# Performance work log

Hardware: AMD Instinct MI355X
Metric: run time of the kernel (lower is better)

## Reference

```python
import jax, jax.numpy as jnp
import numpy as np

DIM = 768
HEADS = 12

def setup_inputs() -> dict:
    key = jax.random.key(0)
    k_x, k_qw, k_qb, k_pw, k_pb = jax.random.split(key, 5)
    x = jax.random.normal(k_x, (4, 2048, DIM), dtype=jnp.float32)
    s = 1.0 / np.sqrt(DIM)
    # torch nn.Linear convention: y = x @ W.T + b, W shape [out, in]
    qkv_w = jax.random.uniform(k_qw, (3 * DIM, DIM), jnp.float32, -s, s)
    qkv_b = jax.random.uniform(k_qb, (3 * DIM,), jnp.float32, -s, s)
    proj_w = jax.random.uniform(k_pw, (DIM, DIM), jnp.float32, -s, s)
    proj_b = jax.random.uniform(k_pb, (DIM,), jnp.float32, -s, s)
    return {"x": x, "qkv_w": qkv_w, "qkv_b": qkv_b, "proj_w": proj_w, "proj_b": proj_b}

def reference(x, qkv_w, qkv_b, proj_w, proj_b):
    B, N, C = x.shape
    H = HEADS
    D = C // H
    scale = D ** -0.5
    qkv = x @ qkv_w.T + qkv_b                      # [B, N, 3C]
    qkv = qkv.reshape(B, N, 3, H, D).transpose(2, 0, 3, 1, 4)  # [3, B, H, N, D]
    q, k, v = qkv[0], qkv[1], qkv[2]
    attn = jnp.einsum('bhnd,bhmd->bhnm', q, k) * scale  # [B, H, N, N]
    attn = jax.nn.softmax(attn, axis=-1)           # dropout p=0.0 -> identity
    out = jnp.einsum('bhnm,bhmd->bhnd', attn, v)   # [B, H, N, D]
    out = out.transpose(0, 2, 1, 3).reshape(B, N, C)
    return out @ proj_w.T + proj_b
```

## Files before the change

kernel.cpp:

```cpp
#include <hip/hip_runtime.h>

#define DIM 768
#define HEADS 12
#define HDIM 64
#define BATCH 4
#define SEQ 2048
#define QSCALE 0.1803368787f
#define MFIX 16.0f
#define QKVSZ ((size_t)BATCH * HEADS * SEQ * HDIM)

typedef __bf16 bf16x8 __attribute__((ext_vector_type(8)));
typedef float  f32x4  __attribute__((ext_vector_type(4)));
typedef float  f32x16 __attribute__((ext_vector_type(16)));
typedef unsigned short u16x8 __attribute__((ext_vector_type(8)));
typedef unsigned short ushort_t;

__device__ inline float exp2_hw(float x){
    float r;
    asm("v_exp_f32 %0, %1\n\ts_nop 0" : "=v"(r) : "v"(x));
    return r;
}
__device__ inline unsigned short f2bf(float x){
    unsigned int u = __float_as_uint(x);
    u += 0x7fffu + ((u >> 16) & 1u);
    return (unsigned short)(u >> 16);
}
__device__ inline unsigned int cvtpk(float lo, float hi){
    unsigned int r;
    asm("v_cvt_pk_bf16_f32 %0, %1, %2" : "=v"(r) : "v"(lo), "v"(hi));
    return r;
}
__device__ inline void gload_lds16(const void* g, void* lds) {
    __builtin_amdgcn_global_load_lds(
        (const __attribute__((address_space(1))) void*)g,
        (__attribute__((address_space(3))) void*)lds, 16, 0, 0);
}

__global__ __launch_bounds__(256) void cvt3(
    const float* __restrict__ s0, ushort_t* __restrict__ d0, int v0,
    const float* __restrict__ s1, ushort_t* __restrict__ d1, int v1,
    const float* __restrict__ s2, ushort_t* __restrict__ d2, int v2)
{
    int idx = blockIdx.x * 256 + threadIdx.x;
    const float* s; ushort_t* d;
    if (idx < v0)           { s = s0; d = d0; }
    else if (idx < v0 + v1) { idx -= v0; s = s1; d = d1; }
    else                    { idx -= v0 + v1; s = s2; d = d2; }
    float4 a = *(const float4*)(s + (size_t)idx * 8);
    float4 b = *(const float4*)(s + (size_t)idx * 8 + 4);
    u16x8 p;
    p[0] = f2bf(a.x); p[1] = f2bf(a.y); p[2] = f2bf(a.z); p[3] = f2bf(a.w);
    p[4] = f2bf(b.x); p[5] = f2bf(b.y); p[6] = f2bf(b.z); p[7] = f2bf(b.w);
    *(u16x8*)(d + (size_t)idx * 8) = p;
}

template <int MODE>
__global__ __launch_bounds__(256) void gemm_mfma(
    const ushort_t* __restrict__ A, const ushort_t* __restrict__ W,
    const float* __restrict__ bias, void* __restrict__ outp,
    int M, int N, int K)
{
    __shared__ ushort_t As[128 * 64];
    __shared__ ushort_t Bs[128 * 64];

    const int tid  = threadIdx.x;
    const int lane = tid & 63;
    const int w    = tid >> 6;
    const int l16  = lane & 15;
    const int lg   = lane >> 4;
    const int wm = w >> 1, wn = w & 1;
    const int m0 = blockIdx.y << 7;
    const int n0 = blockIdx.x << 7;

    const int srow = lane >> 3;
    const int clds = lane & 7;
    const int cg   = clds ^ srow;
    const ushort_t* pA = A + (size_t)(m0 + w * 32 + srow) * K + cg * 8;
    const ushort_t* pB = W + (size_t)(n0 + w * 32 + srow) * K + cg * 8;
    ushort_t* lA = As + (w * 32) * 64;
    ushort_t* lB = Bs + (w * 32) * 64;

    f32x4 acc[4][4];
#pragma unroll
    for (int mi = 0; mi < 4; ++mi)
#pragma unroll
        for (int ni = 0; ni < 4; ++ni) acc[mi][ni] = (f32x4){0.f, 0.f, 0.f, 0.f};

    const int s7  = l16 & 7;
    const int ck0 = (lg ^ s7) << 3;
    const int ck1 = ((4 | lg) ^ s7) << 3;
    const int arow = (wm * 64 + l16) * 64;
    const int brow = (wn * 64 + l16) * 64;

    const int KT = K >> 6;
    for (int kt = 0; kt < KT; ++kt) {
        __syncthreads();
        const ushort_t* ga = pA + kt * 64;
        const ushort_t* gb = pB + kt * 64;
#pragma unroll
        for (int j = 0; j < 4; ++j) {
            gload_lds16(ga + (size_t)j * 8 * K, lA + j * 8 * 64);
            gload_lds16(gb + (size_t)j * 8 * K, lB + j * 8 * 64);
        }
        __syncthreads();

        bf16x8 af[2][4], bfr[2][4];
#pragma unroll
        for (int mi = 0; mi < 4; ++mi) {
            af[0][mi] = *(const bf16x8*)(As + arow + mi * 16 * 64 + ck0);
            af[1][mi] = *(const bf16x8*)(As + arow + mi * 16 * 64 + ck1);
        }
#pragma unroll
        for (int ni = 0; ni < 4; ++ni) {
            bfr[0][ni] = *(const bf16x8*)(Bs + brow + ni * 16 * 64 + ck0);
            bfr[1][ni] = *(const bf16x8*)(Bs + brow + ni * 16 * 64 + ck1);
        }
#pragma unroll
        for (int kk = 0; kk < 2; ++kk)
#pragma unroll
            for (int mi = 0; mi < 4; ++mi)
#pragma unroll
                for (int ni = 0; ni < 4; ++ni)
                    acc[mi][ni] = __builtin_amdgcn_mfma_f32_16x16x32_bf16(
                        af[kk][mi], bfr[kk][ni], acc[mi][ni], 0, 0, 0);
    }

#pragma unroll
    for (int ni = 0; ni < 4; ++ni) {
        const int n = n0 + wn * 64 + ni * 16 + l16;
        const float bv = bias[n];
        if (MODE == 0) {
            float* out = (float*)outp;
#pragma unroll
            for (int mi = 0; mi < 4; ++mi)
#pragma unroll
                for (int r = 0; r < 4; ++r) {
                    const int m = m0 + wm * 64 + mi * 16 + lg * 4 + r;
                    out[(size_t)m * N + n] = acc[mi][ni][r] + bv;
                }
        } else {
            ushort_t* out = (ushort_t*)outp;
            const int which = n / DIM;
            const int rem   = n % DIM;
            const int h = rem >> 6;
            const int d = rem & 63;
            if (which < 2) {
                const float sc = (which == 0) ? QSCALE : 1.0f;
                ushort_t* base = out + (size_t)which * QKVSZ;
#pragma unroll
                for (int mi = 0; mi < 4; ++mi)
#pragma unroll
                    for (int r = 0; r < 4; ++r) {
                        const int m = m0 + wm * 64 + mi * 16 + lg * 4 + r;
                        const int b = m >> 11;
                        const int nrow = m & (SEQ - 1);
                        base[((size_t)(b * HEADS + h) * SEQ + nrow) * HDIM + d] =
                            f2bf((acc[mi][ni][r] + bv) * sc);
                    }
            } else {
                ushort_t* base = out + 2 * QKVSZ;
#pragma unroll
                for (int mi = 0; mi < 4; ++mi) {
                    const int m = m0 + wm * 64 + mi * 16 + lg * 4;
                    const int b = m >> 11;
                    const int nrow = m & (SEQ - 1);
                    ushort4 pk;
                    pk.x = f2bf(acc[mi][ni][0] + bv);
                    pk.y = f2bf(acc[mi][ni][1] + bv);
                    pk.z = f2bf(acc[mi][ni][2] + bv);
                    pk.w = f2bf(acc[mi][ni][3] + bv);
                    *(ushort4*)&base[((size_t)(b * HEADS + h) * HDIM + d) * SEQ + nrow] = pk;
                }
            }
        }
    }
}

__global__ __launch_bounds__(256) void flash_attn_mfma(
    const ushort_t* __restrict__ Qg, const ushort_t* __restrict__ Kg,
    const ushort_t* __restrict__ VTg, ushort_t* __restrict__ Og)
{
    __shared__ ushort_t Ks[2][4096];
    __shared__ ushort_t Vs[2][4096];

    const int tid  = threadIdx.x;
    const int lane = tid & 63;
    const int w    = tid >> 6;
    const int l32  = lane & 31;
    const int hi   = lane >> 5;

    const int L   = blockIdx.x;
    const int swz = (L & 7) * 96 + (L >> 3);
    const int bh  = swz >> 4;
    const int qt  = swz & 15;
    const int q0  = qt * 128 + w * 32;

    const ushort_t* Qp  = Qg + ((size_t)bh * SEQ + q0) * HDIM;
    const ushort_t* Kp  = Kg + (size_t)bh * SEQ * HDIM;
    const ushort_t* VTp = VTg + (size_t)bh * HDIM * SEQ;

    bf16x8 qf[4];
#pragma unroll
    for (int kd = 0; kd < 4; ++kd)
        qf[kd] = *(const bf16x8*)(Qp + l32 * HDIM + kd * 16 + hi * 8);

    bf16x8 ones;
    {
        union { bf16x8 v; unsigned int w4[4]; } u;
        u.w4[0] = u.w4[1] = u.w4[2] = u.w4[3] = 0x3F803F80u;
        ones = u.v;
    }

    f32x16 oacc[2], lacc;
#pragma unroll
    for (int nb = 0; nb < 2; ++nb)
#pragma unroll
        for (int r = 0; r < 16; ++r) oacc[nb][r] = 0.f;
#pragma unroll
    for (int r = 0; r < 16; ++r) lacc[r] = 0.f;

    const int srow = lane >> 3;
    const int clds = lane & 7;
    const int cg   = clds ^ srow;
    const int rw   = w * 16 + srow;

    const ushort_t* gk = Kp + (size_t)rw * HDIM + cg * 8;
    const ushort_t* gv = VTp + (size_t)rw * SEQ + cg * 8;
    ushort_t* lk0 = &Ks[0][0] + w * 1024;
    ushort_t* lv0 = &Vs[0][0] + w * 1024;

    auto stage = [&](int buf) {
        ushort_t* lkb = lk0 + (buf << 12);
        ushort_t* lvb = lv0 + (buf << 12);
        gload_lds16(gk, lkb);
        gload_lds16(gk + 8 * HDIM, lkb + 512);
        gload_lds16(gv, lvb);
        gload_lds16(gv + 8 * SEQ, lvb + 512);
    };

    stage(0);
    gk += 64 * HDIM; gv += 64;
    __syncthreads();

    int cur = 0;
    const int NT = SEQ / 64;
    for (int kt = 0; kt < NT; ++kt) {
        if (kt + 1 < NT) {
            stage(cur ^ 1);
            gk += 64 * HDIM; gv += 64;
        }

        const ushort_t* Kb = &Ks[0][0] + (cur << 12);
        const ushort_t* Vb = &Vs[0][0] + (cur << 12);

#pragma unroll
        for (int b = 0; b < 2; ++b) {
            f32x16 sacc;
#pragma unroll
            for (int r = 0; r < 16; ++r) sacc[r] = -MFIX;
            const int arow = b * 32 + l32;
            const int s7   = l32 & 7;
            __builtin_amdgcn_s_setprio(1);
#pragma unroll
            for (int kd = 0; kd < 4; ++kd) {
                bf16x8 kf = *(const bf16x8*)(Kb + arow * 64 + (((kd * 2 + hi) ^ s7) << 3));
                sacc = __builtin_amdgcn_mfma_f32_32x32x16_bf16(kf, qf[kd], sacc, 0, 0, 0);
            }
            __builtin_amdgcn_s_setprio(0);

            float p[16];
#pragma unroll
            for (int r = 0; r < 16; ++r) p[r] = exp2_hw(sacc[r]);

#pragma unroll
            for (int s = 0; s < 2; ++s) {
                unsigned int x0 = cvtpk(p[8 * s + 0], p[8 * s + 1]);
                unsigned int y0 = cvtpk(p[8 * s + 4], p[8 * s + 5]);
                unsigned int x1 = cvtpk(p[8 * s + 2], p[8 * s + 3]);
                unsigned int y1 = cvtpk(p[8 * s + 6], p[8 * s + 7]);
                asm("v_permlane32_swap_b32 %0, %1" : "+v"(x0), "+v"(y0));
                asm("v_permlane32_swap_b32 %0, %1" : "+v"(x1), "+v"(y1));
                union { bf16x8 v; unsigned int w4[4]; } pa;
                pa.w4[0] = x0; pa.w4[1] = x1; pa.w4[2] = y0; pa.w4[3] = y1;
                const int kc = b * 4 + s * 2 + hi;
                __builtin_amdgcn_s_setprio(1);
                lacc = __builtin_amdgcn_mfma_f32_32x32x16_bf16(pa.v, ones, lacc, 0, 0, 0);
#pragma unroll
                for (int nb = 0; nb < 2; ++nb) {
                    int d = nb * 32 + l32;
                    bf16x8 vf = *(const bf16x8*)(Vb + d * 64 + ((kc ^ (d & 7)) << 3));
                    oacc[nb] = __builtin_amdgcn_mfma_f32_32x32x16_bf16(
                        pa.v, vf, oacc[nb], 0, 0, 0);
                }
                __builtin_amdgcn_s_setprio(0);
            }
        }

        __syncthreads();
        cur ^= 1;
    }

    const int b_ = bh / HEADS;
    const int h_ = bh % HEADS;
    ushort_t* Ob = Og + ((size_t)b_ * SEQ + q0) * DIM + h_ * HDIM;
#pragma unroll
    for (int r = 0; r < 16; ++r) {
        int q = (r & 3) + 8 * (r >> 2) + 4 * hi;
        float li = __builtin_amdgcn_rcpf(lacc[r]);
#pragma unroll
        for (int nb = 0; nb < 2; ++nb)
            Ob[(size_t)q * DIM + nb * 32 + l32] = f2bf(oacc[nb][r] * li);
    }
}

extern "C" void kernel_launch(void* const* d_in, const int* in_sizes, int n_in,
                              void* d_out, int out_size, void* d_ws, size_t ws_size,
                              hipStream_t stream)
{
    const float* x      = (const float*)d_in[0];
    const float* qkv_w  = (const float*)d_in[1];
    const float* qkv_b  = (const float*)d_in[2];
    const float* proj_w = (const float*)d_in[3];
    const float* proj_b = (const float*)d_in[4];
    float* out = (float*)d_out;

    ushort_t* qb     = (ushort_t*)d_ws;
    ushort_t* kb     = qb + QKVSZ;
    ushort_t* vtb    = qb + 2 * QKVSZ;
    ushort_t* attn   = qb + 3 * QKVSZ;
    ushort_t* xb     = qb + 4 * QKVSZ;
    ushort_t* qkvwb  = xb + QKVSZ;
    ushort_t* projwb = qkvwb + (size_t)3 * DIM * DIM;

    const int M = BATCH * SEQ;
    const int NX  = M * DIM;
    const int NQW = 3 * DIM * DIM;
    const int NPW = DIM * DIM;

    cvt3<<<dim3((NX + NQW + NPW) / (8 * 256)), dim3(256), 0, stream>>>(
        x, xb, NX / 8, qkv_w, qkvwb, NQW / 8, proj_w, projwb, NPW / 8);

    dim3 g1(3 * DIM / 128, M / 128);
    gemm_mfma<1><<<g1, dim3(256), 0, stream>>>(xb, qkvwb, qkv_b, (void*)qb, M, 3 * DIM, DIM);

    flash_attn_mfma<<<dim3(768), dim3(256), 0, stream>>>(qb, kb, vtb, attn);

    dim3 g3(DIM / 128, M / 128);
    gemm_mfma<0><<<g3, dim3(256), 0, stream>>>(attn, projwb, proj_b, (void*)out, M, DIM, DIM);
}
```

Measured before the change: 146.4 us.

## Split MFMA accumulators into independent chains and compute row sum on VALU

The QK^T MFMA chain now uses two independent accumulators, and the PV accumulation alternates between two accumulator sets, which shortens dependent MFMA chains. The softmax row-sum MFMA against a ones vector is replaced by a VALU sum of the fp32 exponentials, with a cross-half shuffle and a per-row broadcast at the end. This removes one MFMA per PV step and breaks serial accumulator dependencies, at the cost of more accumulator registers that may reduce occupancy. The row sum is now taken from fp32 values rather than bf16-rounded ones, which slightly changes numerics.

```diff
diff --git a/kernel.cpp b/kernel.cpp
--- a/kernel.cpp
+++ b/kernel.cpp
@@ -204,20 +204,12 @@
     for (int kd = 0; kd < 4; ++kd)
         qf[kd] = *(const bf16x8*)(Qp + l32 * HDIM + kd * 16 + hi * 8);
 
-    bf16x8 ones;
-    {
-        union { bf16x8 v; unsigned int w4[4]; } u;
-        u.w4[0] = u.w4[1] = u.w4[2] = u.w4[3] = 0x3F803F80u;
-        ones = u.v;
-    }
-
-    f32x16 oacc[2], lacc;
+    f32x16 oaccA[2], oaccB[2];
 #pragma unroll
     for (int nb = 0; nb < 2; ++nb)
 #pragma unroll
-        for (int r = 0; r < 16; ++r) oacc[nb][r] = 0.f;
-#pragma unroll
-    for (int r = 0; r < 16; ++r) lacc[r] = 0.f;
+        for (int r = 0; r < 16; ++r) { oaccA[nb][r] = 0.f; oaccB[nb][r] = 0.f; }
+    float lsum = 0.f;
 
     const int srow = lane >> 3;
     const int clds = lane & 7;
@@ -255,22 +247,31 @@
 
 #pragma unroll
         for (int b = 0; b < 2; ++b) {
-            f32x16 sacc;
-#pragma unroll
-            for (int r = 0; r < 16; ++r) sacc[r] = -MFIX;
+            f32x16 sacc0, sacc1;
+#pragma unroll
+            for (int r = 0; r < 16; ++r) { sacc0[r] = -MFIX; sacc1[r] = 0.f; }
             const int arow = b * 32 + l32;
             const int s7   = l32 & 7;
+            bf16x8 kf0 = *(const bf16x8*)(Kb + arow * 64 + (((0 + hi) ^ s7) << 3));
+            bf16x8 kf1 = *(const bf16x8*)(Kb + arow * 64 + (((2 + hi) ^ s7) << 3));
+            bf16x8 kf2 = *(const bf16x8*)(Kb + arow * 64 + (((4 + hi) ^ s7) << 3));
+            bf16x8 kf3 = *(const bf16x8*)(Kb + arow * 64 + (((6 + hi) ^ s7) << 3));
             __builtin_amdgcn_s_setprio(1);
-#pragma unroll
-            for (int kd = 0; kd < 4; ++kd) {
-                bf16x8 kf = *(const bf16x8*)(Kb + arow * 64 + (((kd * 2 + hi) ^ s7) << 3));
-                sacc = __builtin_amdgcn_mfma_f32_32x32x16_bf16(kf, qf[kd], sacc, 0, 0, 0);
-            }
+            sacc0 = __builtin_amdgcn_mfma_f32_32x32x16_bf16(kf0, qf[0], sacc0, 0, 0, 0);
+            sacc1 = __builtin_amdgcn_mfma_f32_32x32x16_bf16(kf1, qf[1], sacc1, 0, 0, 0);
+            sacc0 = __builtin_amdgcn_mfma_f32_32x32x16_bf16(kf2, qf[2], sacc0, 0, 0, 0);
+            sacc1 = __builtin_amdgcn_mfma_f32_32x32x16_bf16(kf3, qf[3], sacc1, 0, 0, 0);
             __builtin_amdgcn_s_setprio(0);
 
             float p[16];
 #pragma unroll
-            for (int r = 0; r < 16; ++r) p[r] = exp2_hw(sacc[r]);
+            for (int r = 0; r < 16; ++r) p[r] = exp2_hw(sacc0[r] + sacc1[r]);
+
+            float t0 = (p[0] + p[1]) + (p[2] + p[3]);
+            float t1 = (p[4] + p[5]) + (p[6] + p[7]);
+            float t2 = (p[8] + p[9]) + (p[10] + p[11]);
+            float t3 = (p[12] + p[13]) + (p[14] + p[15]);
+            lsum += (t0 + t1) + (t2 + t3);
 
 #pragma unroll
             for (int s = 0; s < 2; ++s) {
@@ -284,13 +285,22 @@
                 pa.w4[0] = x0; pa.w4[1] = x1; pa.w4[2] = y0; pa.w4[3] = y1;
                 const int kc = b * 4 + s * 2 + hi;
                 __builtin_amdgcn_s_setprio(1);
-                lacc = __builtin_amdgcn_mfma_f32_32x32x16_bf16(pa.v, ones, lacc, 0, 0, 0);
-#pragma unroll
-                for (int nb = 0; nb < 2; ++nb) {
-                    int d = nb * 32 + l32;
-                    bf16x8 vf = *(const bf16x8*)(Vb + d * 64 + ((kc ^ (d & 7)) << 3));
-                    oacc[nb] = __builtin_amdgcn_mfma_f32_32x32x16_bf16(
-                        pa.v, vf, oacc[nb], 0, 0, 0);
+                if (s == 0) {
+#pragma unroll
+                    for (int nb = 0; nb < 2; ++nb) {
+                        int d = nb * 32 + l32;
+                        bf16x8 vf = *(const bf16x8*)(Vb + d * 64 + ((kc ^ (d & 7)) << 3));
+                        oaccA[nb] = __builtin_amdgcn_mfma_f32_32x32x16_bf16(
+                            pa.v, vf, oaccA[nb], 0, 0, 0);
+                    }
+                } else {
+#pragma unroll
+                    for (int nb = 0; nb < 2; ++nb) {
+                        int d = nb * 32 + l32;
+                        bf16x8 vf = *(const bf16x8*)(Vb + d * 64 + ((kc ^ (d & 7)) << 3));
+                        oaccB[nb] = __builtin_amdgcn_mfma_f32_32x32x16_bf16(
+                            pa.v, vf, oaccB[nb], 0, 0, 0);
+                    }
                 }
                 __builtin_amdgcn_s_setprio(0);
             }
@@ -300,16 +310,19 @@
         cur ^= 1;
     }
 
+    lsum += __shfl_xor(lsum, 32);
+    float linv = 1.0f / lsum;
     const int b_ = bh / HEADS;
     const int h_ = bh % HEADS;
     ushort_t* Ob = Og + ((size_t)b_ * SEQ + q0) * DIM + h_ * HDIM;
 #pragma unroll
     for (int r = 0; r < 16; ++r) {
         int q = (r & 3) + 8 * (r >> 2) + 4 * hi;
-        float li = __builtin_amdgcn_rcpf(lacc[r]);
+        float li = __shfl(linv, q);
 #pragma unroll
         for (int nb = 0; nb < 2; ++nb)
-            Ob[(size_t)q * DIM + nb * 32 + l32] = f2bf(oacc[nb][r] * li);
+            Ob[(size_t)q * DIM + nb * 32 + l32] =
+                f2bf((oaccA[nb][r] + oaccB[nb][r]) * li);
     }
 }
 
```

Result: slower. 180.5 us (+23.3%).

## Split attention KV range in two with partial outputs and a reduce kernel

Applied to the files above, without the earlier changes.

Each attention block now processes half of the key/value sequence, doubling the grid. Unnormalized fp32 partial outputs and row sums go to workspace, and a new kernel sums the two halves, normalizes and writes bf16. The aim is more parallelism and better CU fill. In exchange it adds substantial fp32 partial-output traffic and an extra kernel launch. Summing without rescaling is valid only because a fixed max offset is used.

```diff
diff --git a/kernel.cpp b/kernel.cpp
--- a/kernel.cpp
+++ b/kernel.cpp
@@ -178,7 +178,8 @@
 
 __global__ __launch_bounds__(256) void flash_attn_mfma(
     const ushort_t* __restrict__ Qg, const ushort_t* __restrict__ Kg,
-    const ushort_t* __restrict__ VTg, ushort_t* __restrict__ Og)
+    const ushort_t* __restrict__ VTg,
+    float* __restrict__ pO, float* __restrict__ pL)
 {
     __shared__ ushort_t Ks[2][4096];
     __shared__ ushort_t Vs[2][4096];
@@ -189,11 +190,14 @@
     const int l32  = lane & 31;
     const int hi   = lane >> 5;
 
-    const int L   = blockIdx.x;
-    const int swz = (L & 7) * 96 + (L >> 3);
-    const int bh  = swz >> 4;
-    const int qt  = swz & 15;
-    const int q0  = qt * 128 + w * 32;
+    const int L    = blockIdx.x;
+    const int sq   = L >> 3;
+    const int idx  = (L & 7) * 96 + (sq >> 1);
+    const int half = sq & 1;
+    const int bh   = idx >> 4;
+    const int qt   = idx & 15;
+    const int q0   = qt * 128 + w * 32;
+    const int t0   = half * 16;
 
     const ushort_t* Qp  = Qg + ((size_t)bh * SEQ + q0) * HDIM;
     const ushort_t* Kp  = Kg + (size_t)bh * SEQ * HDIM;
@@ -224,8 +228,8 @@
     const int cg   = clds ^ srow;
     const int rw   = w * 16 + srow;
 
-    const ushort_t* gk = Kp + (size_t)rw * HDIM + cg * 8;
-    const ushort_t* gv = VTp + (size_t)rw * SEQ + cg * 8;
+    const ushort_t* gk = Kp + ((size_t)(t0 * 64) + rw) * HDIM + cg * 8;
+    const ushort_t* gv = VTp + (size_t)rw * SEQ + t0 * 64 + cg * 8;
     ushort_t* lk0 = &Ks[0][0] + w * 1024;
     ushort_t* lv0 = &Vs[0][0] + w * 1024;
 
@@ -243,7 +247,7 @@
     __syncthreads();
 
     int cur = 0;
-    const int NT = SEQ / 64;
+    const int NT = 16;
     for (int kt = 0; kt < NT; ++kt) {
         if (kt + 1 < NT) {
             stage(cur ^ 1);
@@ -300,16 +304,49 @@
         cur ^= 1;
     }
 
-    const int b_ = bh / HEADS;
-    const int h_ = bh % HEADS;
-    ushort_t* Ob = Og + ((size_t)b_ * SEQ + q0) * DIM + h_ * HDIM;
+    float* po = pO + (((size_t)(idx * 2 + half)) << 13) + (w * 32) * 64;
 #pragma unroll
     for (int r = 0; r < 16; ++r) {
         int q = (r & 3) + 8 * (r >> 2) + 4 * hi;
-        float li = __builtin_amdgcn_rcpf(lacc[r]);
 #pragma unroll
         for (int nb = 0; nb < 2; ++nb)
-            Ob[(size_t)q * DIM + nb * 32 + l32] = f2bf(oacc[nb][r] * li);
+            po[q * 64 + nb * 32 + l32] = oacc[nb][r];
+    }
+    if (l32 == 0) {
+        float* pls = pL + (size_t)(idx * 2 + half) * 128 + w * 32;
+#pragma unroll
+        for (int r = 0; r < 16; ++r) {
+            int q = (r & 3) + 8 * (r >> 2) + 4 * hi;
+            pls[q] = lacc[r];
+        }
+    }
+}
+
+__global__ __launch_bounds__(256) void reduce_pair(
+    const float* __restrict__ pO, const float* __restrict__ pL,
+    ushort_t* __restrict__ attn)
+{
+    const int t   = blockIdx.x * 256 + threadIdx.x;
+    const int idx = t >> 7;
+    const int qq  = t & 127;
+    const float* o0 = pO + (((size_t)(idx * 2)) << 13) + qq * 64;
+    const float* o1 = pO + (((size_t)(idx * 2 + 1)) << 13) + qq * 64;
+    const float linv = 1.0f / (pL[(size_t)(idx * 2) * 128 + qq] +
+                               pL[(size_t)(idx * 2 + 1) * 128 + qq]);
+    const int bh = idx >> 4, qt = idx & 15;
+    const int b = bh / HEADS, h = bh % HEADS;
+    const int qrow = qt * 128 + qq;
+    ushort_t* dst = attn + ((size_t)(b * SEQ + qrow)) * DIM + h * 64;
+#pragma unroll
+    for (int d4 = 0; d4 < 16; ++d4) {
+        float4 a = *(const float4*)(o0 + d4 * 4);
+        float4 c = *(const float4*)(o1 + d4 * 4);
+        ushort4 pk;
+        pk.x = f2bf((a.x + c.x) * linv);
+        pk.y = f2bf((a.y + c.y) * linv);
+        pk.z = f2bf((a.z + c.z) * linv);
+        pk.w = f2bf((a.w + c.w) * linv);
+        *(ushort4*)(dst + d4 * 4) = pk;
     }
 }
 
@@ -331,6 +368,8 @@
     ushort_t* xb     = qb + 4 * QKVSZ;
     ushort_t* qkvwb  = xb + QKVSZ;
     ushort_t* projwb = qkvwb + (size_t)3 * DIM * DIM;
+    float*    partO  = (float*)(projwb + (size_t)DIM * DIM);
+    float*    partL  = partO + (size_t)1536 * 8192;
 
     const int M = BATCH * SEQ;
     const int NX  = M * DIM;
@@ -343,7 +382,9 @@
     dim3 g1(3 * DIM / 128, M / 128);
     gemm_mfma<1><<<g1, dim3(256), 0, stream>>>(xb, qkvwb, qkv_b, (void*)qb, M, 3 * DIM, DIM);
 
-    flash_attn_mfma<<<dim3(768), dim3(256), 0, stream>>>(qb, kb, vtb, attn);
+    flash_attn_mfma<<<dim3(1536), dim3(256), 0, stream>>>(qb, kb, vtb, partO, partL);
+
+    reduce_pair<<<dim3(384), dim3(256), 0, stream>>>(partO, partL, attn);
 
     dim3 g3(DIM / 128, M / 128);
     gemm_mfma<0><<<g3, dim3(256), 0, stream>>>(attn, projwb, proj_b, (void*)out, M, DIM, DIM);
```

After: 181.8 us. 1.24x slower.
